# Kernel tuning notes

Hardware: AMD Instinct MI355X
Metric: run time of the kernel (lower is better)

## Reference

```python
import math
import jax, jax.numpy as jnp
import numpy as np

SIZES = [32.0, 64.0, 128.0]
RATIOS = [0.5, 1.0, 2.0]
SCALES = [1.0, 2.0 ** (1.0 / 3.0), 2.0 ** (2.0 / 3.0)]
A = 27            # anchors per location
K = 100           # num_proposals
MIN_BOX = 1.0
IMG = 256.0       # image_size = (256, 256)


def _base_anchors():
    a = []
    for s in SIZES:
        for r in RATIOS:
            for sc in SCALES:
                w = max(s * sc * math.sqrt(r), MIN_BOX)
                h = max(s * sc / math.sqrt(r), MIN_BOX)
                a.append([-w / 2, -h / 2, w / 2, h / 2])
    return jnp.asarray(np.array(a, dtype=np.float32))  # [A, 4]


def _conv(x, w, b, pad):
    y = jax.lax.conv_general_dilated(
        x, w, window_strides=(1, 1), padding=[(pad, pad), (pad, pad)],
        dimension_numbers=("NCHW", "OIHW", "NCHW"))
    return y + b[None, :, None, None]


def _apply_deltas(deltas, anchors):
    # deltas, anchors: [N, M, 4]
    widths = anchors[..., 2] - anchors[..., 0]
    heights = anchors[..., 3] - anchors[..., 1]
    ctr_x = anchors[..., 0] + 0.5 * widths
    ctr_y = anchors[..., 1] + 0.5 * heights
    dx = deltas[..., 0] / 10.0
    dy = deltas[..., 1] / 10.0
    dw = deltas[..., 2] / 5.0
    dh = deltas[..., 3] / 5.0
    pred_ctr_x = dx * widths + ctr_x
    pred_ctr_y = dy * heights + ctr_y
    pred_w = jnp.maximum(jnp.exp(dw) * widths, MIN_BOX)
    pred_h = jnp.maximum(jnp.exp(dh) * heights, MIN_BOX)
    x1 = jnp.clip(pred_ctr_x - 0.5 * pred_w, 0.0, IMG)
    y1 = jnp.clip(pred_ctr_y - 0.5 * pred_h, 0.0, IMG)
    x2 = jnp.clip(pred_ctr_x + 0.5 * pred_w, 0.0, IMG)
    y2 = jnp.clip(pred_ctr_y + 0.5 * pred_h, 0.0, IMG)
    boxes = jnp.stack([x1, y1, x2, y2], axis=-1)
    invalid = ((x2 - x1) < MIN_BOX) | ((y2 - y1) < MIN_BOX)
    return jnp.where(invalid[..., None], anchors, boxes)


def setup_inputs() -> dict:
    key = jax.random.key(0)
    ks = jax.random.split(key, 6)
    N, C, H, W = 8, 256, 64, 64
    return {
        "p4": jax.random.normal(ks[0], (N, C, H, W), jnp.float32),
        "w1": jax.random.normal(ks[1], (C, C, 3, 3), jnp.float32) * 0.02,
        "b1": jnp.zeros((C,), jnp.float32),
        "w2": jax.random.normal(ks[2], (C, C, 3, 3), jnp.float32) * 0.02,
        "b2": jnp.zeros((C,), jnp.float32),
        "wc": jax.random.normal(ks[3], (A, C, 1, 1), jnp.float32) * 0.02,
        "bc": jnp.zeros((A,), jnp.float32),
        "wb": jax.random.normal(ks[4], (4 * A, C, 1, 1), jnp.float32) * 0.02,
        "bb": jnp.zeros((4 * A,), jnp.float32),
    }


def reference(p4, w1, b1, w2, b2, wc, bc, wb, bb):
    feat = jax.nn.relu(_conv(p4, w1, b1, 1))
    feat = jax.nn.relu(_conv(feat, w2, b2, 1))
    logits = _conv(feat, wc, bc, 0)          # [N, A, H, W]
    bbox_deltas = _conv(feat, wb, bb, 0)     # [N, 4A, H, W]

    N, _, H, W = bbox_deltas.shape
    # [N, A, 4, H, W] -> [N, H, W, A, 4] -> [N, HWA, 4]
    deltas = bbox_deltas.reshape(N, A, 4, H, W).transpose(0, 3, 4, 1, 2).reshape(N, -1, 4)
    obj = logits.transpose(0, 2, 3, 1).reshape(N, -1)   # [N, HWA]

    base = _base_anchors()                               # [A, 4]
    shift_x = (jnp.arange(W, dtype=jnp.float32) + 0.5) * (IMG / W)
    shift_y = (jnp.arange(H, dtype=jnp.float32) + 0.5) * (IMG / H)
    sy, sx = jnp.meshgrid(shift_y, shift_x, indexing="ij")   # [H, W]
    shifts = jnp.stack([sx, sy, sx, sy], axis=-1)            # [H, W, 4]
    all_a = base[None, None, :, :] + shifts[:, :, None, :]   # [H, W, A, 4]
    all_a = jnp.maximum(all_a, 0.0)
    all_a = jnp.concatenate([all_a[..., :2], jnp.minimum(all_a[..., 2:], IMG)], axis=-1)
    anchors = jnp.broadcast_to(all_a.reshape(1, -1, 4), (N, H * W * A, 4))

    boxes = _apply_deltas(deltas, anchors)               # [N, HWA, 4]
    valid = ((boxes[..., 2] > boxes[..., 0] + MIN_BOX) &
             (boxes[..., 3] > boxes[..., 1] + MIN_BOX))
    obj = jnp.where(valid, obj, -jnp.inf)
    _, idx = jax.lax.top_k(obj, K)                       # [N, K]
    sel = jnp.take_along_axis(boxes, idx[..., None], axis=1)   # [N, K, 4]
    sel_valid = ((sel[..., 2] > sel[..., 0] + MIN_BOX) &
                 (sel[..., 3] > sel[..., 1] + MIN_BOX))
    bidx = jnp.broadcast_to(
        jnp.arange(N, dtype=sel.dtype)[:, None, None], (N, K, 1))
    props = jnp.concatenate([bidx, sel], axis=-1)        # [N, K, 5]
    # Original compacts variable-length per image; we pad invalid rows with 0
    props = jnp.where(sel_valid[..., None], props, 0.0)
    return props, feat
```

## Files before the change

### kernel.cpp

```cpp
#include <hip/hip_runtime.h>
#include <hip/hip_bf16.h>
#include <math.h>

#define NN 8
#define CH 256
#define HH 64
#define WW 64
#define AA 27
#define KK 100
#define MM (HH * WW * AA)

typedef __attribute__((ext_vector_type(8))) short short8v;
typedef __attribute__((ext_vector_type(4))) float float4v;

#define SPL 8921088ull
#define WSPL 589824ull

#define ABUF_B 25344
#define BBUF_B 73728
#define LDS_TOTAL (2 * ABUF_B + BBUF_B)

__device__ inline void split3(float x, __hip_bfloat16& h, __hip_bfloat16& m,
                              __hip_bfloat16& l)
{
    h = __float2bfloat16(x);
    float r = x - __bfloat162float(h);
    m = __float2bfloat16(r);
    float r2 = r - __bfloat162float(m);
    l = __float2bfloat16(r2);
}

__global__ __launch_bounds__(256)
void prep_misc(__hip_bfloat16* a3, __hip_bfloat16* f1,
               const float* __restrict__ w1, __hip_bfloat16* __restrict__ wt1,
               const float* __restrict__ w2, __hip_bfloat16* __restrict__ wt2)
{
    const int bid = blockIdx.x;
    const int tid = threadIdx.x;
    if (bid < 1560) {
        int g = bid * 256 + tid;
        int arr = g / 66560;
        int rem = g - arr * 66560;
        int n = rem / 8320;
        int rem2 = rem - n * 8320;
        int b = rem2 >> 5;
        int q = rem2 & 31;
        int hp, wp;
        if (b < 66)       { hp = 0;        wp = b; }
        else if (b < 132) { hp = 65;       wp = b - 66; }
        else if (b < 196) { hp = b - 131;  wp = 0; }
        else              { hp = b - 195;  wp = 65; }
        __hip_bfloat16* base = (arr < 3) ? (a3 + (size_t)arr * SPL)
                                         : (f1 + (size_t)(arr - 3) * SPL);
        short8v z = {0, 0, 0, 0, 0, 0, 0, 0};
        *(short8v*)(base + (((size_t)n * 66 + hp) * 66 + wp) * 256 + q * 8) = z;
    } else {
        const bool second = (bid >= 1816);
        const float* w = second ? w2 : w1;
        __hip_bfloat16* wT = second ? wt2 : wt1;
        int t = (bid - (second ? 1816 : 1560)) * 256 + tid;
        int co = t >> 8, ci = t & 255;
        const float* src = w + (size_t)t * 9;
#pragma unroll
        for (int tap = 0; tap < 9; ++tap) {
            __hip_bfloat16 h, m, l;
            split3(src[tap], h, m, l);
            size_t base = ((size_t)tap * 256 + co) * 256 + ci;
            wT[base] = h;
            wT[base + WSPL] = m;
            wT[base + 2 * WSPL] = l;
        }
    }
}

__global__ __launch_bounds__(256)
void prep_in(const float* __restrict__ in, __hip_bfloat16* __restrict__ a3)
{
    __shared__ float s_t[64][65];
    const int tid = threadIdx.x;
    const int ct = blockIdx.x & 3;
    const int row = (blockIdx.x >> 2) & 63;
    const int n = blockIdx.x >> 8;
    const int ci0 = ct * 64;

    for (int i = tid; i < 64 * 64; i += 256) {
        int ci = i >> 6, px = i & 63;
        s_t[ci][px] = in[((size_t)(n * 256 + ci0 + ci) << 12) + (row << 6) + px];
    }
    __syncthreads();
    for (int i = tid; i < 64 * 64; i += 256) {
        int px = i >> 6, ci = i & 63;
        __hip_bfloat16 h, m, l;
        split3(s_t[ci][px], h, m, l);
        size_t base = (((size_t)n * 66 + row + 1) * 66 + px + 1) * 256 + ci0 + ci;
        a3[base] = h;
        a3[base + SPL] = m;
        a3[base + 2 * SPL] = l;
    }
}

typedef __attribute__((address_space(3))) unsigned lds_u32;
typedef const __attribute__((address_space(1))) unsigned glb_u32;

#define AB_PTR(I_)  ((__hip_bfloat16*)(smem + (I_) * ABUF_B))
#define BB_PTR     ((__hip_bfloat16*)(smem + 2 * ABUF_B))

#define STAGE_A(AS_, CI0_, DST_)  do {                                         \
    const __hip_bfloat16* src_ = a3 + (size_t)(AS_) * SPL +                    \
        ((size_t)(n * 66 + rt * 4) * 66) * 256 + (CI0_);                       \
    __hip_bfloat16* dst_ = (DST_);                                             \
    _Pragma("unroll")                                                          \
    for (int it = 0; it < 4; ++it) {                                           \
        int c = it * 512 + tid;                                                \
        if (c < 1584) {                                                        \
            int ph_ = c >> 3;                                                  \
            int x_ = ph_ & 7;                                                  \
            int p_ = ph_ * 2 + (((c >> 2) ^ (x_ >> 2)) & 1);                   \
            int q_ = (c & 3) ^ (x_ & 3);                                       \
            __builtin_amdgcn_global_load_lds(                                  \
                (glb_u32*)(src_ + (size_t)p_ * 256 + q_ * 8),                  \
                (lds_u32*)(dst_ + c * 8), 16, 0, 0);                           \
        }                                                                      \
    }                                                                          \
} while (0)

#define STAGE_B(CI0_)  do {                                                    \
    __hip_bfloat16* dst_ = BB_PTR;                                             \
    _Pragma("unroll")                                                          \
    for (int it = 0; it < 9; ++it) {                                           \
        int c = it * 512 + tid;                                                \
        {                                                                      \
            int tap_ = c >> 9;                                                 \
            int rem_ = c & 511;                                                \
            int ch_ = rem_ >> 3;                                               \
            int x_ = ch_ & 7;                                                  \
            int co_ = ch_ * 2 + (((rem_ >> 2) ^ (x_ >> 2)) & 1);               \
            int q_ = (rem_ & 3) ^ (x_ & 3);                                    \
            __builtin_amdgcn_global_load_lds(                                  \
                (glb_u32*)(wT + (size_t)tap_ * 65536 +                         \
                           (size_t)(co0 + co_) * 256 + (CI0_) + q_ * 8),       \
                (lds_u32*)(dst_ + c * 8), 16, 0, 0);                           \
        }                                                                      \
    }                                                                          \
} while (0)

#define CONV_COMPUTE(NB_, SB_)  do {                                           \
    const __hip_bfloat16* sb_ = (SB_);                                         \
    const __hip_bfloat16* bbp_ = BB_PTR;                                       \
    _Pragma("unroll")                                                          \
    for (int tap = 0; tap < 9; ++tap) {                                        \
        const int dy_ = tap / 3, dx_ = tap % 3;                                \
        const int pA_ = ((w & 3) + dy_) * 66 + dx_ + l15;                      \
        const int aoff_ = ((((pA_ << 2) | l4) ^ ((pA_ >> 1) & 7)) << 3);       \
        short8v af0 = *(const short8v*)(sb_ + aoff_);                          \
        short8v af1 = *(const short8v*)(sb_ + aoff_ + 512);                    \
        short8v af2 = *(const short8v*)(sb_ + aoff_ + 1024);                   \
        short8v af3 = *(const short8v*)(sb_ + aoff_ + 1536);                   \
                   \
        {                                                                      \
            const int coB_ = cohalf * 64 + l15;                                \
            const int boff_ = ((((coB_ << 2) | l4) ^ ((coB_ >> 1) & 7)) << 3); \
            const __hip_bfloat16* bl_ = bbp_ + tap * 4096 + boff_;             \
            short8v b0_ = *(const short8v*)(bl_);                              \
            short8v b1_ = *(const short8v*)(bl_ + 512);                        \
            short8v b2_ = *(const short8v*)(bl_ + 1024);                       \
            short8v b3_ = *(const short8v*)(bl_ + 1536);                       \
            acc[0][0] = __builtin_amdgcn_mfma_f32_16x16x32_bf16(af0, b0_, acc[0][0], 0, 0, 0); \
            acc[1][0] = __builtin_amdgcn_mfma_f32_16x16x32_bf16(af1, b0_, acc[1][0], 0, 0, 0); \
            acc[2][0] = __builtin_amdgcn_mfma_f32_16x16x32_bf16(af2, b0_, acc[2][0], 0, 0, 0); \
            acc[3][0] = __builtin_amdgcn_mfma_f32_16x16x32_bf16(af3, b0_, acc[3][0], 0, 0, 0); \
            acc[0][1] = __builtin_amdgcn_mfma_f32_16x16x32_bf16(af0, b1_, acc[0][1], 0, 0, 0); \
            acc[1][1] = __builtin_amdgcn_mfma_f32_16x16x32_bf16(af1, b1_, acc[1][1], 0, 0, 0); \
            acc[2][1] = __builtin_amdgcn_mfma_f32_16x16x32_bf16(af2, b1_, acc[2][1], 0, 0, 0); \
            acc[3][1] = __builtin_amdgcn_mfma_f32_16x16x32_bf16(af3, b1_, acc[3][1], 0, 0, 0); \
            acc[0][2] = __builtin_amdgcn_mfma_f32_16x16x32_bf16(af0, b2_, acc[0][2], 0, 0, 0); \
            acc[1][2] = __builtin_amdgcn_mfma_f32_16x16x32_bf16(af1, b2_, acc[1][2], 0, 0, 0); \
            acc[2][2] = __builtin_amdgcn_mfma_f32_16x16x32_bf16(af2, b2_, acc[2][2], 0, 0, 0); \
            acc[3][2] = __builtin_amdgcn_mfma_f32_16x16x32_bf16(af3, b2_, acc[3][2], 0, 0, 0); \
            acc[0][3] = __builtin_amdgcn_mfma_f32_16x16x32_bf16(af0, b3_, acc[0][3], 0, 0, 0); \
            acc[1][3] = __builtin_amdgcn_mfma_f32_16x16x32_bf16(af1, b3_, acc[1][3], 0, 0, 0); \
            acc[2][3] = __builtin_amdgcn_mfma_f32_16x16x32_bf16(af2, b3_, acc[2][3], 0, 0, 0); \
            acc[3][3] = __builtin_amdgcn_mfma_f32_16x16x32_bf16(af3, b3_, acc[3][3], 0, 0, 0); \
        }                                                                      \
                                   \
        const __hip_bfloat16* wp_ = wbase + (size_t)(tap * 65536 + ci0);       \
        _Pragma("unroll")                                                      \
        for (int bs = 1; bs < (NB_); ++bs) {                                   \
            const __hip_bfloat16* wq_ = wp_ + (size_t)bs * WSPL;               \
            short8v b0_ = *(const short8v*)(wq_);                              \
            short8v b1_ = *(const short8v*)(wq_ + 4096);                       \
            short8v b2_ = *(const short8v*)(wq_ + 8192);                       \
            short8v b3_ = *(const short8v*)(wq_ + 12288);                      \
            acc[0][0] = __builtin_amdgcn_mfma_f32_16x16x32_bf16(af0, b0_, acc[0][0], 0, 0, 0); \
            acc[1][0] = __builtin_amdgcn_mfma_f32_16x16x32_bf16(af1, b0_, acc[1][0], 0, 0, 0); \
            acc[2][0] = __builtin_amdgcn_mfma_f32_16x16x32_bf16(af2, b0_, acc[2][0], 0, 0, 0); \
            acc[3][0] = __builtin_amdgcn_mfma_f32_16x16x32_bf16(af3, b0_, acc[3][0], 0, 0, 0); \
            acc[0][1] = __builtin_amdgcn_mfma_f32_16x16x32_bf16(af0, b1_, acc[0][1], 0, 0, 0); \
            acc[1][1] = __builtin_amdgcn_mfma_f32_16x16x32_bf16(af1, b1_, acc[1][1], 0, 0, 0); \
            acc[2][1] = __builtin_amdgcn_mfma_f32_16x16x32_bf16(af2, b1_, acc[2][1], 0, 0, 0); \
            acc[3][1] = __builtin_amdgcn_mfma_f32_16x16x32_bf16(af3, b1_, acc[3][1], 0, 0, 0); \
            acc[0][2] = __builtin_amdgcn_mfma_f32_16x16x32_bf16(af0, b2_, acc[0][2], 0, 0, 0); \
            acc[1][2] = __builtin_amdgcn_mfma_f32_16x16x32_bf16(af1, b2_, acc[1][2], 0, 0, 0); \
            acc[2][2] = __builtin_amdgcn_mfma_f32_16x16x32_bf16(af2, b2_, acc[2][2], 0, 0, 0); \
            acc[3][2] = __builtin_amdgcn_mfma_f32_16x16x32_bf16(af3, b2_, acc[3][2], 0, 0, 0); \
            acc[0][3] = __builtin_amdgcn_mfma_f32_16x16x32_bf16(af0, b3_, acc[0][3], 0, 0, 0); \
            acc[1][3] = __builtin_amdgcn_mfma_f32_16x16x32_bf16(af1, b3_, acc[1][3], 0, 0, 0); \
            acc[2][3] = __builtin_amdgcn_mfma_f32_16x16x32_bf16(af2, b3_, acc[2][3], 0, 0, 0); \
            acc[3][3] = __builtin_amdgcn_mfma_f32_16x16x32_bf16(af3, b3_, acc[3][3], 0, 0, 0); \
        }                                                                      \
    }                                                                          \
} while (0)

template <int MODE>
__global__ __launch_bounds__(512, 1)
void conv_mfma(const __hip_bfloat16* __restrict__ a3,
               const __hip_bfloat16* __restrict__ wT,
               const float* __restrict__ bias,
               __hip_bfloat16* __restrict__ outb,
               float* __restrict__ outf)
{
    extern __shared__ __align__(16) char smem[];

    const int tid = threadIdx.x;
    const int lane = tid & 63, w = tid >> 6;
    const int l15 = lane & 15, l4 = lane >> 4;
    const int cohalf = w >> 2;
    const int bid = blockIdx.x;
    const int cg = bid & 1, rt = (bid >> 1) & 15, n = bid >> 5;
    const int co0 = cg * 128;
    const int row = rt * 4 + (w & 3);

    float4v acc[4][4];
#pragma unroll
    for (int p = 0; p < 4; ++p)
#pragma unroll
        for (int q = 0; q < 4; ++q) acc[p][q] = (float4v){0.f, 0.f, 0.f, 0.f};

    const __hip_bfloat16* wbase = wT + ((size_t)(co0 + cohalf * 64 + l15)) * 256 + l4 * 8;

    STAGE_A(0, 0, AB_PTR(0));
    STAGE_B(0);
    __syncthreads();

    int cur = 0;
    for (int chunk = 0; chunk < 8; ++chunk) {
        const int ci0 = chunk * 32;
        STAGE_A(1, ci0, AB_PTR(cur ^ 1));
        CONV_COMPUTE(3, AB_PTR(cur));
        __syncthreads();
        cur ^= 1;
        STAGE_A(2, ci0, AB_PTR(cur ^ 1));
        CONV_COMPUTE(2, AB_PTR(cur));
        __syncthreads();
        cur ^= 1;
        if (chunk < 7) STAGE_A(0, ci0 + 32, AB_PTR(cur ^ 1));
        CONV_COMPUTE(1, AB_PTR(cur));
        __syncthreads();
        if (chunk < 7) {
            STAGE_B(ci0 + 32);
            __syncthreads();
        }
        cur ^= 1;
    }

    float bco[4];
#pragma unroll
    for (int q = 0; q < 4; ++q) bco[q] = bias[co0 + cohalf * 64 + q * 16 + l15];

    if (MODE == 0) {
#pragma unroll
        for (int p = 0; p < 4; ++p)
#pragma unroll
            for (int q = 0; q < 4; ++q) {
#pragma unroll
                for (int v = 0; v < 4; ++v) {
                    float y = fmaxf(acc[p][q][v] + bco[q], 0.f);
                    __hip_bfloat16 h, m, l;
                    split3(y, h, m, l);
                    size_t base = (((size_t)n * 66 + row + 1) * 66 +
                                   p * 16 + l4 * 4 + v + 1) * 256 +
                                  co0 + cohalf * 64 + q * 16 + l15;
                    outb[base] = h;
                    outb[base + SPL] = m;
                    outb[base + 2 * SPL] = l;
                }
            }
    } else {
#pragma unroll
        for (int p = 0; p < 4; ++p)
#pragma unroll
            for (int q = 0; q < 4; ++q) {
                float4v y;
#pragma unroll
                for (int v = 0; v < 4; ++v) y[v] = fmaxf(acc[p][q][v] + bco[q], 0.f);
                *(float4v*)(outf + ((size_t)(n * 256 + co0 + cohalf * 64 + q * 16 + l15) << 12) +
                            row * 64 + p * 16 + l4 * 4) = y;
            }
    }
}

__global__ __launch_bounds__(256, 2)
void conv1x1_kernel(const float* __restrict__ feat, const float* __restrict__ wc,
                    const float* __restrict__ bc, const float* __restrict__ wb,
                    const float* __restrict__ bb, float* __restrict__ tmp)
{
    __shared__ float s_f[64][64];
    __shared__ float s_w[64][137];

    const int tid  = threadIdx.x;
    const int n    = blockIdx.x >> 6;
    const int px0  = (blockIdx.x & 63) << 6;
    const int lane = tid & 63;
    const int g    = tid >> 6;

    float acc[34];
#pragma unroll
    for (int k = 0; k < 34; ++k) acc[k] = 0.f;

    for (int chb = 0; chb < 4; ++chb) {
        const int ci0 = chb << 6;
        __syncthreads();
        for (int i = tid; i < 64 * 64; i += 256) {
            int ci = i >> 6, pp = i & 63;
            s_f[ci][pp] = feat[(((size_t)n * CH + ci0 + ci) << 12) + px0 + pp];
        }
        for (int i = tid; i < 135 * 64; i += 256) {
            int co = i >> 6, ci = i & 63;
            float wv = (co < 27) ? wc[(size_t)co * CH + ci0 + ci]
                                 : wb[(size_t)(co - 27) * CH + ci0 + ci];
            s_w[ci][co] = wv;
        }
        __syncthreads();
        for (int ci = 0; ci < 64; ++ci) {
            float f = s_f[ci][lane];
#pragma unroll
            for (int k = 0; k < 34; ++k) {
                int co = g * 34 + k;
                acc[k] += f * s_w[ci][co < 135 ? co : 134];
            }
        }
    }
#pragma unroll
    for (int k = 0; k < 34; ++k) {
        int co = g * 34 + k;
        if (co < 135) {
            float b = (co < 27) ? bc[co] : bb[co - 27];
            tmp[((size_t)n * 135 + co) * 4096 + px0 + lane] = acc[k] + b;
        }
    }
}

__global__ void boxes_kernel(const float* __restrict__ tmp,
                             float* __restrict__ scores, float* __restrict__ boxes)
{
    const int n = blockIdx.y;
    const int i = blockIdx.x * 256 + threadIdx.x;
    const int a = i >> 12;
    const int p = i & 4095;

    const float* t = tmp + (size_t)n * 135 * 4096;
    float logit = t[(size_t)a * 4096 + p];
    float d0 = t[((size_t)(27 + a * 4 + 0)) * 4096 + p];
    float d1 = t[((size_t)(27 + a * 4 + 1)) * 4096 + p];
    float d2 = t[((size_t)(27 + a * 4 + 2)) * 4096 + p];
    float d3 = t[((size_t)(27 + a * 4 + 3)) * 4096 + p];

    const int hh = p >> 6, ww = p & 63;
    const int si = a / 9, ri = (a / 3) % 3, sci = a % 3;

    double s  = (si == 0) ? 32.0 : (si == 1 ? 64.0 : 128.0);
    double r  = (ri == 0) ? 0.5 : (ri == 1 ? 1.0 : 2.0);
    double sv = (sci == 0) ? 1.0 : (sci == 1 ? pow(2.0, 1.0 / 3.0) : pow(2.0, 2.0 / 3.0));
    double sq = sqrt(r);
    float wa = (float)fmax(s * sv * sq, 1.0);
    float ha = (float)fmax(s * sv / sq, 1.0);
    float bx1 = -0.5f * wa, by1 = -0.5f * ha, bx2 = 0.5f * wa, by2 = 0.5f * ha;

    float sx = ((float)ww + 0.5f) * 4.0f;
    float sy = ((float)hh + 0.5f) * 4.0f;
    float ax1 = fmaxf(bx1 + sx, 0.f);
    float ay1 = fmaxf(by1 + sy, 0.f);
    float ax2 = fminf(fmaxf(bx2 + sx, 0.f), 256.f);
    float ay2 = fminf(fmaxf(by2 + sy, 0.f), 256.f);

    float wdt = ax2 - ax1, hgt = ay2 - ay1;
    float cx = ax1 + 0.5f * wdt, cy = ay1 + 0.5f * hgt;
    float dx = d0 / 10.f, dy = d1 / 10.f, dw = d2 / 5.f, dh = d3 / 5.f;
    float pcx = dx * wdt + cx, pcy = dy * hgt + cy;
    float pw = fmaxf(expf(dw) * wdt, 1.f);
    float ph = fmaxf(expf(dh) * hgt, 1.f);
    float x1 = fminf(fmaxf(pcx - 0.5f * pw, 0.f), 256.f);
    float y1 = fminf(fmaxf(pcy - 0.5f * ph, 0.f), 256.f);
    float x2 = fminf(fmaxf(pcx + 0.5f * pw, 0.f), 256.f);
    float y2 = fminf(fmaxf(pcy + 0.5f * ph, 0.f), 256.f);

    bool inval = ((x2 - x1) < 1.f) || ((y2 - y1) < 1.f);
    float fx1 = inval ? ax1 : x1, fy1 = inval ? ay1 : y1;
    float fx2 = inval ? ax2 : x2, fy2 = inval ? ay2 : y2;
    bool valid = (fx2 > fx1 + 1.f) && (fy2 > fy1 + 1.f);

    const int m = p * 27 + a;
    scores[(size_t)n * MM + m] = valid ? logit : -INFINITY;
    float4 bx = make_float4(fx1, fy1, fx2, fy2);
    *(float4*)&boxes[((size_t)n * MM + m) * 4] = bx;
}

__device__ inline unsigned ordf(float f)
{
    unsigned u = __float_as_uint(f);
    return (u & 0x80000000u) ? ~u : (u | 0x80000000u);
}

__global__ void topk_props(const float* __restrict__ scores,
                           const float* __restrict__ boxes,
                           float* __restrict__ props)
{
    const int n = blockIdx.x;
    const int tid = threadIdx.x;
    const float* sc = scores + (size_t)n * MM;

    __shared__ unsigned hist[256];
    __shared__ unsigned u_prefix, u_need, cnt;
    __shared__ unsigned long long selk[100];
    __shared__ unsigned wave_tot[16];

    if (tid == 0) { u_prefix = 0; u_need = 100; cnt = 0; }
    __syncthreads();

    for (int pass = 0; pass < 4; ++pass) {
        if (tid < 256) hist[tid] = 0;
        __syncthreads();
        unsigned pf = u_prefix;
        int shift = 24 - pass * 8;
        for (int i4 = tid; i4 < MM / 4; i4 += 1024) {
            float4 v = ((const float4*)sc)[i4];
#pragma unroll
            for (int k = 0; k < 4; ++k) {
                float f = (k == 0) ? v.x : (k == 1) ? v.y : (k == 2) ? v.z : v.w;
                unsigned o = ordf(f);
                bool match = (pass == 0) || ((o >> (shift + 8)) == (pf >> (shift + 8)));
                if (match) atomicAdd(&hist[(o >> shift) & 255u], 1u);
            }
        }
        __syncthreads();
        if (tid == 0) {
            unsigned nd = u_need;
            int b = 255;
            for (;;) {
                unsigned cb = hist[b];
                if (nd <= cb || b == 0) break;
                nd -= cb;
                --b;
            }
            u_need = nd;
            u_prefix = pf | ((unsigned)b << shift);
        }
        __syncthreads();
    }
    const unsigned T = u_prefix;
    const int need = (int)u_need;
    const int cgt = 100 - need;

    for (int i4 = tid; i4 < MM / 4; i4 += 1024) {
        float4 v = ((const float4*)sc)[i4];
#pragma unroll
        for (int k = 0; k < 4; ++k) {
            float f = (k == 0) ? v.x : (k == 1) ? v.y : (k == 2) ? v.z : v.w;
            unsigned o = ordf(f);
            if (o > T) {
                unsigned pz = atomicAdd(&cnt, 1u);
                selk[pz] = ((unsigned long long)o << 32) |
                           (unsigned long long)(~(unsigned)(i4 * 4 + k));
            }
        }
    }
    __syncthreads();

    unsigned hv = 0;
    for (int base = 0; base < MM; base += 1024) {
        int i = base + tid;
        unsigned o = ordf(sc[i]);
        bool f = (o == T);
        unsigned long long bal = __ballot(f);
        if ((tid & 63) == 0) wave_tot[tid >> 6] = (unsigned)__popcll(bal);
        __syncthreads();
        unsigned wbase = 0, tot = 0;
        int wv = tid >> 6;
        for (int w2 = 0; w2 < 16; ++w2) {
            unsigned cw = wave_tot[w2];
            tot += cw;
            if (w2 < wv) wbase += cw;
        }
        if (f) {
            unsigned rk = hv + wbase +
                          (unsigned)__popcll(bal & ((1ull << (tid & 63)) - 1ull));
            if (rk < (unsigned)need)
                selk[cgt + rk] =
                    ((unsigned long long)o << 32) | (unsigned long long)(~(unsigned)i);
        }
        hv += tot;
        __syncthreads();
        if (hv >= (unsigned)need) break;
    }
    __syncthreads();

    if (tid < 100) {
        unsigned long long k = selk[tid];
        int rank = 0;
        for (int j = 0; j < 100; ++j) rank += (selk[j] > k) ? 1 : 0;
        unsigned idx = ~(unsigned)(k & 0xFFFFFFFFull);
        const float* bx = boxes + ((size_t)n * MM + idx) * 4;
        float x1 = bx[0], y1 = bx[1], x2 = bx[2], y2 = bx[3];
        bool v = (x2 > x1 + 1.f) && (y2 > y1 + 1.f);
        float* o = props + ((size_t)n * 100 + rank) * 5;
        o[0] = v ? (float)n : 0.f;
        o[1] = v ? x1 : 0.f;
        o[2] = v ? y1 : 0.f;
        o[3] = v ? x2 : 0.f;
        o[4] = v ? y2 : 0.f;
    }
}

extern "C" void kernel_launch(void* const* d_in, const int* in_sizes, int n_in,
                              void* d_out, int out_size, void* d_ws, size_t ws_size,
                              hipStream_t stream)
{
    const float* p4 = (const float*)d_in[0];
    const float* w1 = (const float*)d_in[1];
    const float* b1 = (const float*)d_in[2];
    const float* w2 = (const float*)d_in[3];
    const float* b2 = (const float*)d_in[4];
    const float* wc = (const float*)d_in[5];
    const float* bc = (const float*)d_in[6];
    const float* wb = (const float*)d_in[7];
    const float* bb = (const float*)d_in[8];

    float* out   = (float*)d_out;
    float* props = out;
    float* feat  = out + 4000;

    char* ws = (char*)d_ws;
    __hip_bfloat16* a3p = (__hip_bfloat16*)ws;
    __hip_bfloat16* f1p = (__hip_bfloat16*)(ws + 53526528);
    __hip_bfloat16* wt1 = (__hip_bfloat16*)(ws + 107053056);
    __hip_bfloat16* wt2 = (__hip_bfloat16*)(ws + 110592000);
    float* tmp    = (float*)ws;
    float* scores = (float*)(ws + 17694720);
    float* boxesb = (float*)(ws + 21233664);

    prep_misc<<<2072, 256, 0, stream>>>(a3p, f1p, w1, wt1, w2, wt2);
    prep_in<<<2048, 256, 0, stream>>>(p4, a3p);
    conv_mfma<0><<<256, 512, LDS_TOTAL, stream>>>(a3p, wt1, b1, f1p, nullptr);
    conv_mfma<1><<<256, 512, LDS_TOTAL, stream>>>(f1p, wt2, b2, nullptr, feat);
    conv1x1_kernel<<<512, 256, 0, stream>>>(feat, wc, bc, wb, bb, tmp);
    dim3 g2(432, 8);
    boxes_kernel<<<g2, 256, 0, stream>>>(tmp, scores, boxesb);
    topk_props<<<8, 1024, 0, stream>>>(scores, boxesb, props);
}
```

Before: 770.6 us.

## Load conv weight fragments directly into registers instead of staging in LDS

The weight (B) operand of the 3x3 conv is no longer staged through a 72 KB LDS buffer. Each wave now loads its 9x4 bf16 fragments straight from global memory into registers at the start of each input-channel chunk. This removes the B staging copies, one barrier per chunk and most of the LDS footprint, which could allow more blocks per CU. In exchange each wave holds 36 short8 vectors (144 VGPRs) and issues direct global loads whose latency is not overlapped with compute, so it risks register pressure and stalls.

```diff
diff --git a/kernel.cpp b/kernel.cpp
--- a/kernel.cpp
+++ b/kernel.cpp
@@ -17,8 +17,7 @@
 #define WSPL 589824ull
 
 #define ABUF_B 25344
-#define BBUF_B 73728
-#define LDS_TOTAL (2 * ABUF_B + BBUF_B)
+#define LDS_TOTAL (2 * ABUF_B)
 
 __device__ inline void split3(float x, __hip_bfloat16& h, __hip_bfloat16& m,
                               __hip_bfloat16& l)
@@ -103,7 +102,6 @@
 typedef const __attribute__((address_space(1))) unsigned glb_u32;
 
 #define AB_PTR(I_)  ((__hip_bfloat16*)(smem + (I_) * ABUF_B))
-#define BB_PTR     ((__hip_bfloat16*)(smem + 2 * ABUF_B))
 
 #define STAGE_A(AS_, CI0_, DST_)  do {                                         \
     const __hip_bfloat16* src_ = a3 + (size_t)(AS_) * SPL +                    \
@@ -124,29 +122,8 @@
     }                                                                          \
 } while (0)
 
-#define STAGE_B(CI0_)  do {                                                    \
-    __hip_bfloat16* dst_ = BB_PTR;                                             \
-    _Pragma("unroll")                                                          \
-    for (int it = 0; it < 9; ++it) {                                           \
-        int c = it * 512 + tid;                                                \
-        {                                                                      \
-            int tap_ = c >> 9;                                                 \
-            int rem_ = c & 511;                                                \
-            int ch_ = rem_ >> 3;                                               \
-            int x_ = ch_ & 7;                                                  \
-            int co_ = ch_ * 2 + (((rem_ >> 2) ^ (x_ >> 2)) & 1);               \
-            int q_ = (rem_ & 3) ^ (x_ & 3);                                    \
-            __builtin_amdgcn_global_load_lds(                                  \
-                (glb_u32*)(wT + (size_t)tap_ * 65536 +                         \
-                           (size_t)(co0 + co_) * 256 + (CI0_) + q_ * 8),       \
-                (lds_u32*)(dst_ + c * 8), 16, 0, 0);                           \
-        }                                                                      \
-    }                                                                          \
-} while (0)
-
 #define CONV_COMPUTE(NB_, SB_)  do {                                           \
     const __hip_bfloat16* sb_ = (SB_);                                         \
-    const __hip_bfloat16* bbp_ = BB_PTR;                                       \
     _Pragma("unroll")                                                          \
     for (int tap = 0; tap < 9; ++tap) {                                        \
         const int dy_ = tap / 3, dx_ = tap % 3;                                \
@@ -156,15 +133,12 @@
         short8v af1 = *(const short8v*)(sb_ + aoff_ + 512);                    \
         short8v af2 = *(const short8v*)(sb_ + aoff_ + 1024);                   \
         short8v af3 = *(const short8v*)(sb_ + aoff_ + 1536);                   \
-                   \
+                 \
         {                                                                      \
-            const int coB_ = cohalf * 64 + l15;                                \
-            const int boff_ = ((((coB_ << 2) | l4) ^ ((coB_ >> 1) & 7)) << 3); \
-            const __hip_bfloat16* bl_ = bbp_ + tap * 4096 + boff_;             \
-            short8v b0_ = *(const short8v*)(bl_);                              \
-            short8v b1_ = *(const short8v*)(bl_ + 512);                        \
-            short8v b2_ = *(const short8v*)(bl_ + 1024);                       \
-            short8v b3_ = *(const short8v*)(bl_ + 1536);                       \
+            short8v b0_ = bh[tap][0];                                          \
+            short8v b1_ = bh[tap][1];                                          \
+            short8v b2_ = bh[tap][2];                                          \
+            short8v b3_ = bh[tap][3];                                          \
             acc[0][0] = __builtin_amdgcn_mfma_f32_16x16x32_bf16(af0, b0_, acc[0][0], 0, 0, 0); \
             acc[1][0] = __builtin_amdgcn_mfma_f32_16x16x32_bf16(af1, b0_, acc[1][0], 0, 0, 0); \
             acc[2][0] = __builtin_amdgcn_mfma_f32_16x16x32_bf16(af2, b0_, acc[2][0], 0, 0, 0); \
@@ -239,12 +213,22 @@
     const __hip_bfloat16* wbase = wT + ((size_t)(co0 + cohalf * 64 + l15)) * 256 + l4 * 8;
 
     STAGE_A(0, 0, AB_PTR(0));
-    STAGE_B(0);
     __syncthreads();
 
     int cur = 0;
     for (int chunk = 0; chunk < 8; ++chunk) {
         const int ci0 = chunk * 32;
+
+        short8v bh[9][4];
+#pragma unroll
+        for (int tap = 0; tap < 9; ++tap) {
+            const __hip_bfloat16* wp_ = wbase + (size_t)(tap * 65536 + ci0);
+            bh[tap][0] = *(const short8v*)(wp_);
+            bh[tap][1] = *(const short8v*)(wp_ + 4096);
+            bh[tap][2] = *(const short8v*)(wp_ + 8192);
+            bh[tap][3] = *(const short8v*)(wp_ + 12288);
+        }
+
         STAGE_A(1, ci0, AB_PTR(cur ^ 1));
         CONV_COMPUTE(3, AB_PTR(cur));
         __syncthreads();
@@ -256,10 +240,6 @@
         if (chunk < 7) STAGE_A(0, ci0 + 32, AB_PTR(cur ^ 1));
         CONV_COMPUTE(1, AB_PTR(cur));
         __syncthreads();
-        if (chunk < 7) {
-            STAGE_B(ci0 + 32);
-            __syncthreads();
-        }
         cur ^= 1;
     }
 
```

After: 1.021 ms. 1.32x slower.
